# Performance work log

Measured on AMD Instinct MI355X. Metric: run time of the kernel, lower is better.

## Reference

```python
import jax, jax.numpy as jnp
import numpy as np

EPS = 1e-10
BETA = 1.0


def setup_inputs() -> dict:
    key = jax.random.key(0)
    k1, k2 = jax.random.split(key)
    N, C = 2097152, 32
    logits = jax.random.normal(k1, (N, C), dtype=jnp.float32)
    labels = jax.random.randint(k2, (N,), 0, C, dtype=jnp.int64)
    unc_th = jnp.float32(1.0)
    return {"logits": logits, "labels": labels, "unc_th": unc_th}


def reference(logits, labels, unc_th):
    # probs: [N, C]
    probs = jax.nn.softmax(logits, axis=1)
    confidences = jnp.max(probs, axis=1)            # [N]
    predictions = jnp.argmax(probs, axis=1)         # [N]
    # predictive entropy (type=0 path): [N]
    unc = -jnp.sum(probs * jnp.log(probs + EPS), axis=-1)

    accurate = labels == predictions                 # [N] bool
    certain = unc <= unc_th                          # [N] bool
    t = jnp.tanh(unc)

    zero = jnp.zeros((), dtype=probs.dtype)
    n_ac = jnp.sum(jnp.where(accurate & certain, confidences * (1.0 - t), zero))
    n_au = jnp.sum(jnp.where(accurate & ~certain, confidences * t, zero))
    n_ic = jnp.sum(jnp.where(~accurate & certain, (1.0 - confidences) * (1.0 - t), zero))
    n_iu = jnp.sum(jnp.where(~accurate & ~certain, (1.0 - confidences) * t, zero))

    avu = (n_ac + n_iu) / (n_ac + n_au + n_ic + n_iu + EPS)
    avu_loss = -BETA * jnp.log(avu + EPS)
    return jnp.reshape(avu_loss, (1,))
```

## Files before the change

### kernel.cpp

```cpp
#include <hip/hip_runtime.h>
#include <math.h>


__global__ __launch_bounds__(256) void avu_main(
    const float* __restrict__ logits,
    const int* __restrict__ labels,
    const float* __restrict__ unc_th_p,
    float4* __restrict__ partials,
    int N)
{
    const float unc_th = unc_th_p[0];
    const float4* __restrict__ p4 = (const float4*)logits;

    const int lane = threadIdx.x & 63;
    const int wave = threadIdx.x >> 6;
    const int sub  = lane & 7;
    const int rgrp = lane >> 3;

    const int wavesPerBlock = blockDim.x >> 6;
    const int W  = blockIdx.x * wavesPerBlock + wave;
    const int TW = gridDim.x * wavesPerBlock;

    const int G   = (N + 7) >> 3;
    const int gpw = (G + TW - 1) / TW;
    const int g0  = W * gpw;

    const int totalF4 = N * 8;

    float acc0 = 0.f, acc1 = 0.f, acc2 = 0.f, acc3 = 0.f;

    float4 v = make_float4(0.f, 0.f, 0.f, 0.f);
    if (g0 < G) {
        const int f4 = g0 * 64 + lane;
        if (f4 < totalF4) v = p4[f4];
    }

    for (int i = 0; i < gpw; ++i) {
        const int g = g0 + i;
        if (g >= G) break;

        float4 vn = make_float4(0.f, 0.f, 0.f, 0.f);
        if (i + 1 < gpw && g + 1 < G) {
            const int f4 = (g + 1) * 64 + lane;
            if (f4 < totalF4) vn = p4[f4];
        }

        const int row   = (g << 3) + rgrp;
        const bool valid = (row < N);
        const int lab = valid ? labels[row] : -1;

        const int base = sub << 2;
        float m = v.x; int mi = base;
        if (v.y > m) { m = v.y; mi = base + 1; }
        if (v.z > m) { m = v.z; mi = base + 2; }
        if (v.w > m) { m = v.w; mi = base + 3; }

#pragma unroll
        for (int mask = 1; mask <= 4; mask <<= 1) {
            const float om = __shfl_xor(m, mask);
            const int   oi = __shfl_xor(mi, mask);
            if (om > m || (om == m && oi < mi)) { m = om; mi = oi; }
        }

        const float d0 = v.x - m, d1 = v.y - m, d2 = v.z - m, d3 = v.w - m;
        const float e0 = __expf(d0), e1 = __expf(d1);
        const float e2 = __expf(d2), e3 = __expf(d3);
        float S   = (e0 + e1) + (e2 + e3);
        float dot = (e0 * d0 + e1 * d1) + (e2 * d2 + e3 * d3);
#pragma unroll
        for (int mask = 1; mask <= 4; mask <<= 1) {
            S   += __shfl_xor(S, mask);
            dot += __shfl_xor(dot, mask);
        }

        const float rS   = 1.0f / S;
        const float conf = rS;
        const float unc  = __logf(S) - dot * rS;
        const float t = 1.0f - 2.0f / (__expf(2.0f * unc) + 1.0f);

        const bool accurate = (lab == mi);
        const bool certain  = (unc <= unc_th);

        const float a = accurate ? conf : (1.0f - conf);
        const float w = certain ? (1.0f - t) : t;
        float val = a * w;
        val = (sub == 0 && valid) ? val : 0.f;

        acc0 += ( accurate &&  certain) ? val : 0.f;
        acc1 += ( accurate && !certain) ? val : 0.f;
        acc2 += (!accurate &&  certain) ? val : 0.f;
        acc3 += (!accurate && !certain) ? val : 0.f;

        v = vn;
    }

#pragma unroll
    for (int mask = 1; mask <= 32; mask <<= 1) {
        acc0 += __shfl_xor(acc0, mask);
        acc1 += __shfl_xor(acc1, mask);
        acc2 += __shfl_xor(acc2, mask);
        acc3 += __shfl_xor(acc3, mask);
    }

    __shared__ float4 red[4];
    if (lane == 0) red[wave] = make_float4(acc0, acc1, acc2, acc3);
    __syncthreads();

    if (threadIdx.x == 0) {
        float4 r = red[0];
        for (int w2 = 1; w2 < wavesPerBlock; ++w2) {
            const float4 q = red[w2];
            r.x += q.x; r.y += q.y; r.z += q.z; r.w += q.w;
        }
        partials[blockIdx.x] = r;
    }
}

__global__ __launch_bounds__(64) void avu_final(
    const float4* __restrict__ partials, int nPart,
    float* __restrict__ out)
{
    double s0 = 0.0, s1 = 0.0, s2 = 0.0, s3 = 0.0;
    for (int i = threadIdx.x; i < nPart; i += 64) {
        const float4 p = partials[i];
        s0 += (double)p.x; s1 += (double)p.y;
        s2 += (double)p.z; s3 += (double)p.w;
    }
#pragma unroll
    for (int mask = 1; mask <= 32; mask <<= 1) {
        s0 += __shfl_xor(s0, mask);
        s1 += __shfl_xor(s1, mask);
        s2 += __shfl_xor(s2, mask);
        s3 += __shfl_xor(s3, mask);
    }
    if (threadIdx.x == 0) {
        const double avu = (s0 + s3) / (s0 + s1 + s2 + s3 + 1e-10);
        out[0] = (float)(-log(avu + 1e-10));
    }
}

extern "C" void kernel_launch(void* const* d_in, const int* in_sizes, int n_in,
                              void* d_out, int out_size, void* d_ws, size_t ws_size,
                              hipStream_t stream)
{
    const float* logits = (const float*)d_in[0];
    const int*   labels = (const int*)d_in[1];
    const float* unc_th = (const float*)d_in[2];
    float*       out    = (float*)d_out;
    float4*      parts  = (float4*)d_ws;

    const int N = in_sizes[1];
    const int BLOCKS = 2048;

    avu_main<<<BLOCKS, 256, 0, stream>>>(logits, labels, unc_th, parts, N);
    avu_final<<<1, 64, 0, stream>>>(parts, BLOCKS, out);
}
```

Before: 376.8 us.

## Deepen prefetch to four stages with nontemporal loads and bounds-free specialization

Replaces the single-step prefetch with a four-deep register ring of logits and labels, so each wave has more memory requests in flight. Loads use nontemporal hints, and a template specialization drops the bounds checks when N divides evenly across the waves. The intent is to hide HBM latency on this bandwidth-bound streaming reduction, at the cost of more registers per thread, which could lower occupancy.

After: 404.8 us. 7.4% more time.

```diff
diff --git a/kernel.cpp b/kernel.cpp
--- a/kernel.cpp
+++ b/kernel.cpp
@@ -2,6 +2,9 @@
 #include <math.h>
 
 
+typedef float f32x4 __attribute__((ext_vector_type(4)));
+
+template<bool EXACT>
 __global__ __launch_bounds__(256) void avu_main(
     const float* __restrict__ logits,
     const int* __restrict__ labels,
@@ -10,7 +13,7 @@
     int N)
 {
     const float unc_th = unc_th_p[0];
-    const float4* __restrict__ p4 = (const float4*)logits;
+    const f32x4* __restrict__ p4 = (const f32x4*)logits;
 
     const int lane = threadIdx.x & 63;
     const int wave = threadIdx.x >> 6;
@@ -22,38 +25,49 @@
     const int TW = gridDim.x * wavesPerBlock;
 
     const int G   = (N + 7) >> 3;
-    const int gpw = (G + TW - 1) / TW;
+    const int gpw = EXACT ? (G / TW) : ((G + TW - 1) / TW);
     const int g0  = W * gpw;
-
-    const int totalF4 = N * 8;
 
     float acc0 = 0.f, acc1 = 0.f, acc2 = 0.f, acc3 = 0.f;
 
-    float4 v = make_float4(0.f, 0.f, 0.f, 0.f);
-    if (g0 < G) {
-        const int f4 = g0 * 64 + lane;
-        if (f4 < totalF4) v = p4[f4];
+    f32x4 v[4];
+    int   lab[4];
+#pragma unroll
+    for (int j = 0; j < 4; ++j) {
+        const int g = g0 + j;
+        if (EXACT || (g < G && j < gpw)) {
+            v[j]   = __builtin_nontemporal_load(&p4[(size_t)g * 64 + lane]);
+            const int row = (g << 3) + rgrp;
+            lab[j] = (EXACT || row < N) ? labels[row] : -1;
+        } else {
+            v[j] = (f32x4){0.f, 0.f, 0.f, 0.f};
+            lab[j] = -1;
+        }
     }
 
     for (int i = 0; i < gpw; ++i) {
         const int g = g0 + i;
-        if (g >= G) break;
+        if (!EXACT && g >= G) break;
 
-        float4 vn = make_float4(0.f, 0.f, 0.f, 0.f);
-        if (i + 1 < gpw && g + 1 < G) {
-            const int f4 = (g + 1) * 64 + lane;
-            if (f4 < totalF4) vn = p4[f4];
+        const int j = i & 3;
+        const f32x4 cv  = v[j];
+        const int   clab = lab[j];
+
+        const int gn = g + 4;
+        if ((i + 4 < gpw) && (EXACT || gn < G)) {
+            v[j] = __builtin_nontemporal_load(&p4[(size_t)gn * 64 + lane]);
+            const int rown = (gn << 3) + rgrp;
+            lab[j] = (EXACT || rown < N) ? labels[rown] : -1;
         }
 
         const int row   = (g << 3) + rgrp;
-        const bool valid = (row < N);
-        const int lab = valid ? labels[row] : -1;
+        const bool valid = EXACT || (row < N);
 
         const int base = sub << 2;
-        float m = v.x; int mi = base;
-        if (v.y > m) { m = v.y; mi = base + 1; }
-        if (v.z > m) { m = v.z; mi = base + 2; }
-        if (v.w > m) { m = v.w; mi = base + 3; }
+        float m = cv.x; int mi = base;
+        if (cv.y > m) { m = cv.y; mi = base + 1; }
+        if (cv.z > m) { m = cv.z; mi = base + 2; }
+        if (cv.w > m) { m = cv.w; mi = base + 3; }
 
 #pragma unroll
         for (int mask = 1; mask <= 4; mask <<= 1) {
@@ -62,7 +76,7 @@
             if (om > m || (om == m && oi < mi)) { m = om; mi = oi; }
         }
 
-        const float d0 = v.x - m, d1 = v.y - m, d2 = v.z - m, d3 = v.w - m;
+        const float d0 = cv.x - m, d1 = cv.y - m, d2 = cv.z - m, d3 = cv.w - m;
         const float e0 = __expf(d0), e1 = __expf(d1);
         const float e2 = __expf(d2), e3 = __expf(d3);
         float S   = (e0 + e1) + (e2 + e3);
@@ -78,7 +92,7 @@
         const float unc  = __logf(S) - dot * rS;
         const float t = 1.0f - 2.0f / (__expf(2.0f * unc) + 1.0f);
 
-        const bool accurate = (lab == mi);
+        const bool accurate = (clab == mi);
         const bool certain  = (unc <= unc_th);
 
         const float a = accurate ? conf : (1.0f - conf);
@@ -90,8 +104,6 @@
         acc1 += ( accurate && !certain) ? val : 0.f;
         acc2 += (!accurate &&  certain) ? val : 0.f;
         acc3 += (!accurate && !certain) ? val : 0.f;
-
-        v = vn;
     }
 
 #pragma unroll
@@ -151,7 +163,14 @@
 
     const int N = in_sizes[1];
     const int BLOCKS = 2048;
+    const int TW = BLOCKS * (256 / 64);
+    const int G  = (N + 7) >> 3;
 
-    avu_main<<<BLOCKS, 256, 0, stream>>>(logits, labels, unc_th, parts, N);
+    const bool exact = ((N & 7) == 0) && (G % TW == 0);
+    if (exact) {
+        avu_main<true><<<BLOCKS, 256, 0, stream>>>(logits, labels, unc_th, parts, N);
+    } else {
+        avu_main<false><<<BLOCKS, 256, 0, stream>>>(logits, labels, unc_th, parts, N);
+    }
     avu_final<<<1, 64, 0, stream>>>(parts, BLOCKS, out);
 }
```

## Transpose logits through LDS so each lane processes a full row

Applied to the files above, without the earlier changes.

Adds a main kernel that loads 64 rows per wave with coalesced float4 loads, stages them in LDS, and reads them back rotated so each lane holds one full 32-wide row. This removes the per-row cross-lane shuffle reductions for max and sums and checks accuracy by comparing the label's logit to the max instead of tracking argmax. Grid size is halved, and a simple row-per-thread fallback covers shapes that do not tile evenly. The extra LDS round-trip and higher register use may lower occupancy, and ties at the max are treated differently from argmax.

After: 372.0 us. About the same (-1.3%).

```diff
diff --git a/kernel.cpp b/kernel.cpp
--- a/kernel.cpp
+++ b/kernel.cpp
@@ -2,7 +2,121 @@
 #include <math.h>
 
 
-__global__ __launch_bounds__(256) void avu_main(
+typedef float f32x4 __attribute__((ext_vector_type(4)));
+
+__global__ __launch_bounds__(256) void avu_lds(
+    const float* __restrict__ logits,
+    const int* __restrict__ labels,
+    const float* __restrict__ unc_th_p,
+    float4* __restrict__ partials,
+    int tilesPerWave)
+{
+    const float unc_th = unc_th_p[0];
+    const f32x4* __restrict__ p4 = (const f32x4*)logits;
+
+    __shared__ f32x4 lds4[2048];
+
+    const int lane = threadIdx.x & 63;
+    const int wave = threadIdx.x >> 6;
+    const int wavesPerBlock = blockDim.x >> 6;
+    const int W = blockIdx.x * wavesPerBlock + wave;
+
+    f32x4* __restrict__ wbuf = &lds4[wave << 9];
+
+    float acc0 = 0.f, acc1 = 0.f, acc2 = 0.f, acc3 = 0.f;
+
+    const int t0 = W * tilesPerWave;
+    for (int i = 0; i < tilesPerWave; ++i) {
+        const int tile = t0 + i;
+        const size_t base4 = (size_t)tile << 9;
+
+        const int lab = labels[(tile << 6) + lane];
+
+        f32x4 tmp[8];
+#pragma unroll
+        for (int k = 0; k < 8; ++k)
+            tmp[k] = p4[base4 + (k << 6) + lane];
+#pragma unroll
+        for (int k = 0; k < 8; ++k)
+            wbuf[(k << 6) + lane] = tmp[k];
+
+        f32x4 rv[8];
+#pragma unroll
+        for (int s = 0; s < 8; ++s) {
+            const int g = (s + lane) & 7;
+            rv[s] = wbuf[(lane << 3) + g];
+        }
+
+        float pm[8];
+#pragma unroll
+        for (int s = 0; s < 8; ++s)
+            pm[s] = fmaxf(fmaxf(rv[s].x, rv[s].y), fmaxf(rv[s].z, rv[s].w));
+        const float m = fmaxf(fmaxf(fmaxf(pm[0], pm[1]), fmaxf(pm[2], pm[3])),
+                              fmaxf(fmaxf(pm[4], pm[5]), fmaxf(pm[6], pm[7])));
+
+        const int sl = ((lab >> 2) - lane) & 7;
+        const int el = lab & 3;
+        f32x4 vsel = rv[0];
+#pragma unroll
+        for (int s = 1; s < 8; ++s)
+            if (sl == s) vsel = rv[s];
+        const float c01  = (el & 1) ? vsel.y : vsel.x;
+        const float c23  = (el & 1) ? vsel.w : vsel.z;
+        const float x_lab = (el & 2) ? c23 : c01;
+
+        float S = 0.f, dot = 0.f;
+#pragma unroll
+        for (int s = 0; s < 8; ++s) {
+            const float d0 = rv[s].x - m, d1 = rv[s].y - m;
+            const float d2 = rv[s].z - m, d3 = rv[s].w - m;
+            const float e0 = __expf(d0), e1 = __expf(d1);
+            const float e2 = __expf(d2), e3 = __expf(d3);
+            S   += (e0 + e1) + (e2 + e3);
+            dot += (e0 * d0 + e1 * d1) + (e2 * d2 + e3 * d3);
+        }
+
+        const float rS   = 1.0f / S;
+        const float conf = rS;
+        const float unc  = __logf(S) - dot * rS;
+        const float t    = 1.0f - 2.0f / (__expf(2.0f * unc) + 1.0f);
+
+        const bool accurate = (x_lab == m);
+        const bool certain  = (unc <= unc_th);
+
+        const float a = accurate ? conf : (1.0f - conf);
+        const float w = certain ? (1.0f - t) : t;
+        const float val = a * w;
+
+        acc0 += ( accurate &&  certain) ? val : 0.f;
+        acc1 += ( accurate && !certain) ? val : 0.f;
+        acc2 += (!accurate &&  certain) ? val : 0.f;
+        acc3 += (!accurate && !certain) ? val : 0.f;
+    }
+
+#pragma unroll
+    for (int mask = 1; mask <= 32; mask <<= 1) {
+        acc0 += __shfl_xor(acc0, mask);
+        acc1 += __shfl_xor(acc1, mask);
+        acc2 += __shfl_xor(acc2, mask);
+        acc3 += __shfl_xor(acc3, mask);
+    }
+
+    __shared__ float4 red[4];
+    __syncthreads();
+    if (lane == 0) red[wave] = make_float4(acc0, acc1, acc2, acc3);
+    __syncthreads();
+
+    if (threadIdx.x == 0) {
+        float4 r = red[0];
+        for (int w2 = 1; w2 < wavesPerBlock; ++w2) {
+            const float4 q = red[w2];
+            r.x += q.x; r.y += q.y; r.z += q.z; r.w += q.w;
+        }
+        partials[blockIdx.x] = r;
+    }
+}
+
+__global__ __launch_bounds__(256) void avu_fallback(
     const float* __restrict__ logits,
     const int* __restrict__ labels,
     const float* __restrict__ unc_th_p,
@@ -10,90 +124,30 @@
     int N)
 {
     const float unc_th = unc_th_p[0];
-    const float4* __restrict__ p4 = (const float4*)logits;
-
-    const int lane = threadIdx.x & 63;
-    const int wave = threadIdx.x >> 6;
-    const int sub  = lane & 7;
-    const int rgrp = lane >> 3;
-
-    const int wavesPerBlock = blockDim.x >> 6;
-    const int W  = blockIdx.x * wavesPerBlock + wave;
-    const int TW = gridDim.x * wavesPerBlock;
-
-    const int G   = (N + 7) >> 3;
-    const int gpw = (G + TW - 1) / TW;
-    const int g0  = W * gpw;
-
-    const int totalF4 = N * 8;
-
     float acc0 = 0.f, acc1 = 0.f, acc2 = 0.f, acc3 = 0.f;
-
-    float4 v = make_float4(0.f, 0.f, 0.f, 0.f);
-    if (g0 < G) {
-        const int f4 = g0 * 64 + lane;
-        if (f4 < totalF4) v = p4[f4];
-    }
-
-    for (int i = 0; i < gpw; ++i) {
-        const int g = g0 + i;
-        if (g >= G) break;
-
-        float4 vn = make_float4(0.f, 0.f, 0.f, 0.f);
-        if (i + 1 < gpw && g + 1 < G) {
-            const int f4 = (g + 1) * 64 + lane;
-            if (f4 < totalF4) vn = p4[f4];
-        }
-
-        const int row   = (g << 3) + rgrp;
-        const bool valid = (row < N);
-        const int lab = valid ? labels[row] : -1;
-
-        const int base = sub << 2;
-        float m = v.x; int mi = base;
-        if (v.y > m) { m = v.y; mi = base + 1; }
-        if (v.z > m) { m = v.z; mi = base + 2; }
-        if (v.w > m) { m = v.w; mi = base + 3; }
-
-#pragma unroll
-        for (int mask = 1; mask <= 4; mask <<= 1) {
-            const float om = __shfl_xor(m, mask);
-            const int   oi = __shfl_xor(mi, mask);
-            if (om > m || (om == m && oi < mi)) { m = om; mi = oi; }
-        }
-
-        const float d0 = v.x - m, d1 = v.y - m, d2 = v.z - m, d3 = v.w - m;
-        const float e0 = __expf(d0), e1 = __expf(d1);
-        const float e2 = __expf(d2), e3 = __expf(d3);
-        float S   = (e0 + e1) + (e2 + e3);
-        float dot = (e0 * d0 + e1 * d1) + (e2 * d2 + e3 * d3);
-#pragma unroll
-        for (int mask = 1; mask <= 4; mask <<= 1) {
-            S   += __shfl_xor(S, mask);
-            dot += __shfl_xor(dot, mask);
-        }
-
-        const float rS   = 1.0f / S;
-        const float conf = rS;
-        const float unc  = __logf(S) - dot * rS;
+    const int stride = gridDim.x * blockDim.x;
+    for (int row = blockIdx.x * blockDim.x + threadIdx.x; row < N; row += stride) {
+        const float* x = logits + (size_t)row * 32;
+        float m = x[0]; int mi = 0;
+        for (int c = 1; c < 32; ++c) { const float v = x[c]; if (v > m) { m = v; mi = c; } }
+        float S = 0.f, dot = 0.f;
+        for (int c = 0; c < 32; ++c) {
+            const float d = x[c] - m; const float e = __expf(d);
+            S += e; dot += e * d;
+        }
+        const float rS = 1.0f / S;
+        const float unc = __logf(S) - dot * rS;
         const float t = 1.0f - 2.0f / (__expf(2.0f * unc) + 1.0f);
-
-        const bool accurate = (lab == mi);
-        const bool certain  = (unc <= unc_th);
-
-        const float a = accurate ? conf : (1.0f - conf);
+        const bool accurate = (labels[row] == mi);
+        const bool certain = (unc <= unc_th);
+        const float a = accurate ? rS : (1.0f - rS);
         const float w = certain ? (1.0f - t) : t;
-        float val = a * w;
-        val = (sub == 0 && valid) ? val : 0.f;
-
+        const float val = a * w;
         acc0 += ( accurate &&  certain) ? val : 0.f;
         acc1 += ( accurate && !certain) ? val : 0.f;
         acc2 += (!accurate &&  certain) ? val : 0.f;
         acc3 += (!accurate && !certain) ? val : 0.f;
-
-        v = vn;
-    }
-
+    }
 #pragma unroll
     for (int mask = 1; mask <= 32; mask <<= 1) {
         acc0 += __shfl_xor(acc0, mask);
@@ -101,14 +155,13 @@
         acc2 += __shfl_xor(acc2, mask);
         acc3 += __shfl_xor(acc3, mask);
     }
-
     __shared__ float4 red[4];
-    if (lane == 0) red[wave] = make_float4(acc0, acc1, acc2, acc3);
+    const int wave = threadIdx.x >> 6;
+    if ((threadIdx.x & 63) == 0) red[wave] = make_float4(acc0, acc1, acc2, acc3);
     __syncthreads();
-
     if (threadIdx.x == 0) {
         float4 r = red[0];
-        for (int w2 = 1; w2 < wavesPerBlock; ++w2) {
+        for (int w2 = 1; w2 < (int)(blockDim.x >> 6); ++w2) {
             const float4 q = red[w2];
             r.x += q.x; r.y += q.y; r.z += q.z; r.w += q.w;
         }
@@ -150,8 +203,15 @@
     float4*      parts  = (float4*)d_ws;
 
     const int N = in_sizes[1];
-    const int BLOCKS = 2048;
-
-    avu_main<<<BLOCKS, 256, 0, stream>>>(logits, labels, unc_th, parts, N);
+    const int BLOCKS = 1024;
+    const int TW = BLOCKS * 4;
+
+    const int tiles = N >> 6;
+    if ((N & 63) == 0 && tiles % TW == 0) {
+        avu_lds<<<BLOCKS, 256, 0, stream>>>(logits, labels, unc_th, parts,
+                                            tiles / TW);
+    } else {
+        avu_fallback<<<BLOCKS, 256, 0, stream>>>(logits, labels, unc_th, parts, N);
+    }
     avu_final<<<1, 64, 0, stream>>>(parts, BLOCKS, out);
 }
```
